# Optimization experiments

Hardware: AMD Instinct MI355X
Metric: run time of the kernel (lower is better)

Reference implementation:

```python
import jax, jax.numpy as jnp
import numpy as np

B, C_LOW, C_HIGH, KC, VC, H, W = 4, 512, 256, 64, 64, 64, 64


def setup_inputs() -> dict:
    key = jax.random.key(0)
    ks = jax.random.split(key, 6)
    x_low = jax.random.normal(ks[0], (B, C_LOW, H, W), dtype=jnp.float32)
    x_high = jax.random.normal(ks[1], (B, C_HIGH, H, W), dtype=jnp.float32)
    # 1x1 conv weights, fan-in scaled
    Wq = jax.random.normal(ks[2], (KC, C_HIGH), dtype=jnp.float32) / np.sqrt(C_HIGH)
    Wk = jax.random.normal(ks[3], (KC, C_LOW), dtype=jnp.float32) / np.sqrt(C_LOW)
    Wv = jax.random.normal(ks[4], (VC, C_LOW), dtype=jnp.float32) / np.sqrt(C_LOW)
    Wo = jax.random.normal(ks[5], (C_HIGH, VC), dtype=jnp.float32) / np.sqrt(VC)
    return {
        "x_low": x_low, "x_high": x_high,
        "Wq": Wq, "bq": jnp.zeros((KC,), jnp.float32),
        "Wk": Wk, "bk": jnp.zeros((KC,), jnp.float32),
        "Wv": Wv, "bv": jnp.zeros((VC,), jnp.float32),
        "Wo": Wo, "bo": jnp.zeros((C_HIGH,), jnp.float32),
    }


def reference(x_low, x_high, Wq, bq, Wk, bk, Wv, bv, Wo, bo):
    b, ch, h, w = x_high.shape
    n = h * w  # tokens per image
    # 1x1 convs == per-pixel linear maps; flatten spatial to tokens
    xh = x_high.reshape(b, ch, n)                # [B, C_high, N]
    xl = x_low.reshape(b, x_low.shape[1], n)     # [B, C_low,  N]
    q = jnp.einsum('kc,bcn->bnk', Wq, xh) + bq   # [B, N, KC]
    k = jnp.einsum('kc,bcn->bkn', Wk, xl) + bk[:, None]  # [B, KC, N]
    v = jnp.einsum('vc,bcn->bnv', Wv, xl) + bv   # [B, N, VC]
    sim = jnp.einsum('bnk,bkm->bnm', q, k)       # [B, N, N]
    attn = jax.nn.softmax(sim, axis=-1)
    ctx = jnp.einsum('bnm,bmv->bnv', attn, v)    # [B, N, VC]
    out = jnp.einsum('ov,bnv->bon', Wo, ctx) + bo[:, None]  # [B, C_high, N]
    return out.reshape(b, ch, h, w) + x_high
```

## Files before the change

### kernel.cpp

```cpp
#include <hip/hip_runtime.h>
#include <hip/hip_bf16.h>
#include <math.h>
#include <stdint.h>

#define B 4
#define CLOW 512
#define CHIGH 256
#define KC 64
#define VC 64
#define N 4096

typedef __attribute__((ext_vector_type(8))) short bf16x8;
typedef __attribute__((ext_vector_type(4))) short bf16x4;
typedef __attribute__((ext_vector_type(4))) float f32x4;

__device__ inline unsigned short f2bf(float f) {
    union { float f; uint32_t u; } v; v.f = f;
    uint32_t u = v.u;
    u += 0x7fff + ((u >> 16) & 1);
    return (unsigned short)(u >> 16);
}
__device__ inline float bf2f(unsigned short h) {
    union { uint32_t u; float f; } v; v.u = ((uint32_t)h) << 16;
    return v.f;
}
__device__ inline uint32_t packbf2(float a, float b) {
    union { __hip_bfloat16 h; unsigned short u; } ca, cb;
    ca.h = __float2bfloat16(a);
    cb.h = __float2bfloat16(b);
    return (uint32_t)ca.u | ((uint32_t)cb.u << 16);
}

#if __has_builtin(__builtin_amdgcn_exp2f)
#define EXP2(x) __builtin_amdgcn_exp2f(x)
#else
#define EXP2(x) exp2f(x)
#endif


__global__ __launch_bounds__(256) void proj_mfma(
    const float* __restrict__ xl, const float* __restrict__ xh,
    const float* __restrict__ Wq, const float* __restrict__ bq,
    const float* __restrict__ Wk, const float* __restrict__ bk,
    const float* __restrict__ Wv, const float* __restrict__ bv,
    unsigned short* __restrict__ Qt, unsigned short* __restrict__ Kt,
    unsigned short* __restrict__ Vt)
{
    const int proj = blockIdx.z;
    const int b    = blockIdx.y;
    const int n0   = blockIdx.x * 64;
    const int tid  = threadIdx.x;
    const int wv   = tid >> 6;
    const int lane = tid & 63;
    const int lo   = lane & 15;
    const int hi   = lane >> 4;
    const int hi8  = hi * 8;

    __shared__ unsigned short XtHi[64][40];
    __shared__ unsigned short XtLo[64][40];

    const int cR = tid >> 3;
    const int t8 = (tid & 7) * 8;

    const size_t kqFragOff = (size_t)((((wv*2 + (hi>>1)) & 3)*16 + lo)*8 + (hi&1)*4);

    if (proj == 0) {
        f32x4 acc[4];
        #pragma unroll
        for (int t = 0; t < 4; ++t)
            #pragma unroll
            for (int r = 0; r < 4; ++r) acc[t][r] = bq[wv*16 + hi*4 + r];

        for (int c0 = 0; c0 < CHIGH; c0 += 32) {
            const float* src = xh + ((size_t)b*CHIGH + c0 + cR)*N + n0 + t8;
            float4 v0 = *(const float4*)src;
            float4 v1 = *(const float4*)(src + 4);
            float vv[8] = {v0.x, v0.y, v0.z, v0.w, v1.x, v1.y, v1.z, v1.w};
            #pragma unroll
            for (int i = 0; i < 8; ++i) {
                unsigned short h = f2bf(vv[i]);
                XtHi[t8 + i][cR] = h;
                XtLo[t8 + i][cR] = f2bf(vv[i] - bf2f(h));
            }
            __syncthreads();

            const float* wp = Wq + (size_t)(wv*16 + lo)*CHIGH + c0 + hi8;
            float4 w0 = *(const float4*)wp;
            float4 w1 = *(const float4*)(wp + 4);
            float ww[8] = {w0.x, w0.y, w0.z, w0.w, w1.x, w1.y, w1.z, w1.w};
            bf16x8 ah, al;
            #pragma unroll
            for (int i = 0; i < 8; ++i) {
                unsigned short h = f2bf(ww[i]);
                ah[i] = (short)h;
                al[i] = (short)f2bf(ww[i] - bf2f(h));
            }

            #pragma unroll
            for (int t = 0; t < 4; ++t) {
                bf16x8 xhv = *(const bf16x8*)&XtHi[t*16 + lo][hi8];
                bf16x8 xlv = *(const bf16x8*)&XtLo[t*16 + lo][hi8];
                acc[t] = __builtin_amdgcn_mfma_f32_16x16x32_bf16(ah, xhv, acc[t], 0, 0, 0);
                acc[t] = __builtin_amdgcn_mfma_f32_16x16x32_bf16(ah, xlv, acc[t], 0, 0, 0);
                acc[t] = __builtin_amdgcn_mfma_f32_16x16x32_bf16(al, xhv, acc[t], 0, 0, 0);
            }
            __syncthreads();
        }
        const float qs = 1.4426950408889634f;
        #pragma unroll
        for (int t = 0; t < 4; ++t) {
            bf16x4 o;
            #pragma unroll
            for (int r = 0; r < 4; ++r) o[r] = (short)f2bf(acc[t][r] * qs);
            size_t base = (((size_t)b*256 + (n0>>4) + t)*2 + (wv>>1))*512;
            *(bf16x4*)&Qt[base + kqFragOff] = o;
        }
    } else {
        f32x4 accK[4], accV[4];
        #pragma unroll
        for (int t = 0; t < 4; ++t)
            #pragma unroll
            for (int r = 0; r < 4; ++r) {
                accK[t][r] = bk[wv*16 + hi*4 + r];
                accV[t][r] = bv[wv*16 + hi*4 + r];
            }

        for (int c0 = 0; c0 < CLOW; c0 += 32) {
            const float* src = xl + ((size_t)b*CLOW + c0 + cR)*N + n0 + t8;
            float4 v0 = *(const float4*)src;
            float4 v1 = *(const float4*)(src + 4);
            float vv[8] = {v0.x, v0.y, v0.z, v0.w, v1.x, v1.y, v1.z, v1.w};
            #pragma unroll
            for (int i = 0; i < 8; ++i) {
                unsigned short h = f2bf(vv[i]);
                XtHi[t8 + i][cR] = h;
                XtLo[t8 + i][cR] = f2bf(vv[i] - bf2f(h));
            }
            __syncthreads();

            const float* wpk = Wk + (size_t)(wv*16 + lo)*CLOW + c0 + hi8;
            const float* wpv = Wv + (size_t)(wv*16 + lo)*CLOW + c0 + hi8;
            bf16x8 ahk, alk, ahv, alv;
            {
                float4 w0 = *(const float4*)wpk;
                float4 w1 = *(const float4*)(wpk + 4);
                float ww[8] = {w0.x,w0.y,w0.z,w0.w,w1.x,w1.y,w1.z,w1.w};
                #pragma unroll
                for (int i = 0; i < 8; ++i) {
                    unsigned short h = f2bf(ww[i]);
                    ahk[i] = (short)h;
                    alk[i] = (short)f2bf(ww[i] - bf2f(h));
                }
            }
            {
                float4 w0 = *(const float4*)wpv;
                float4 w1 = *(const float4*)(wpv + 4);
                float ww[8] = {w0.x,w0.y,w0.z,w0.w,w1.x,w1.y,w1.z,w1.w};
                #pragma unroll
                for (int i = 0; i < 8; ++i) {
                    unsigned short h = f2bf(ww[i]);
                    ahv[i] = (short)h;
                    alv[i] = (short)f2bf(ww[i] - bf2f(h));
                }
            }

            #pragma unroll
            for (int t = 0; t < 4; ++t) {
                bf16x8 xhv = *(const bf16x8*)&XtHi[t*16 + lo][hi8];
                bf16x8 xlv = *(const bf16x8*)&XtLo[t*16 + lo][hi8];
                accK[t] = __builtin_amdgcn_mfma_f32_16x16x32_bf16(ahk, xhv, accK[t], 0, 0, 0);
                accK[t] = __builtin_amdgcn_mfma_f32_16x16x32_bf16(ahk, xlv, accK[t], 0, 0, 0);
                accK[t] = __builtin_amdgcn_mfma_f32_16x16x32_bf16(alk, xhv, accK[t], 0, 0, 0);
                accV[t] = __builtin_amdgcn_mfma_f32_16x16x32_bf16(ahv, xhv, accV[t], 0, 0, 0);
                accV[t] = __builtin_amdgcn_mfma_f32_16x16x32_bf16(ahv, xlv, accV[t], 0, 0, 0);
                accV[t] = __builtin_amdgcn_mfma_f32_16x16x32_bf16(alv, xhv, accV[t], 0, 0, 0);
            }
            __syncthreads();
        }

        #pragma unroll
        for (int t = 0; t < 4; ++t) {
            bf16x4 o;
            #pragma unroll
            for (int r = 0; r < 4; ++r) o[r] = (short)f2bf(accK[t][r]);
            size_t kbase = (((size_t)b*256 + (n0>>4) + t)*2 + (wv>>1))*512;
            *(bf16x4*)&Kt[kbase + kqFragOff] = o;

            const int kvtile = (n0 >> 5) + (t >> 1);
            const int hi_f   = (t & 1)*2 + (lo >> 3);
            size_t vbase = ((size_t)b*128 + kvtile)*2048 + (size_t)wv*512
                         + (size_t)hi_f*128 + (size_t)(lo & 7);
            #pragma unroll
            for (int r = 0; r < 4; ++r)
                Vt[vbase + (size_t)(hi*4 + r)*8] = f2bf(accV[t][r]);
        }
    }
}

#define WSPLIT 8
#define QT 4
__global__ __launch_bounds__(512) void attn(
    const unsigned short* __restrict__ Qt,
    const unsigned short* __restrict__ Kt,
    const unsigned short* __restrict__ Vt,
    float* __restrict__ ctx)
{
    const int bid = blockIdx.x;
    const int xcd = bid & 7;
    const int b   = xcd >> 1;
    const int q0  = ((bid >> 3) * 2 + (xcd & 1)) * 64;

    const int tid  = threadIdx.x;
    const int wv   = tid >> 6;
    const int lane = tid & 63;
    const int lo   = lane & 15;
    const int hi   = lane >> 4;

    __shared__ float Olds[WSPLIT][64][68];
    __shared__ float llds[WSPLIT][64];

    const unsigned short* Kb = Kt + (size_t)b*N*KC;
    const unsigned short* Vb = Vt + (size_t)b*VC*N;
    const unsigned short* Qb = Qt + (size_t)b*N*KC;

    bf16x8 qf[2][QT];
    #pragma unroll
    for (int qt = 0; qt < QT; ++qt) {
        #pragma unroll
        for (int kt = 0; kt < 2; ++kt)
            qf[kt][qt] = *(const bf16x8*)&Qb[(((size_t)(q0>>4) + qt)*2 + kt)*512 + lane*8];
    }

    f32x4 O[4][QT] = {};
    float l_run[QT] = {};

    const int kv0   = wv * (N/WSPLIT);
    const int kvend = kv0 + (N/WSPLIT);

    for (int kv = kv0; kv < kvend; kv += 32) {
        bf16x8 ka[2][2], va[4];
        #pragma unroll
        for (int j = 0; j < 2; ++j)
            #pragma unroll
            for (int m = 0; m < 2; ++m)
                ka[j][m] = *(const bf16x8*)&Kb[(((size_t)(kv>>4) + j)*2 + m)*512 + lane*8];
        #pragma unroll
        for (int vt = 0; vt < 4; ++vt)
            va[vt] = *(const bf16x8*)&Vb[((size_t)(kv>>5))*2048 + vt*512 + lane*8];

        #pragma unroll
        for (int qt = 0; qt < QT; ++qt) {
            f32x4 st[2];
            #pragma unroll
            for (int j = 0; j < 2; ++j) {
                f32x4 z = {};
                z     = __builtin_amdgcn_mfma_f32_16x16x32_bf16(ka[j][0], qf[0][qt], z, 0, 0, 0);
                st[j] = __builtin_amdgcn_mfma_f32_16x16x32_bf16(ka[j][1], qf[1][qt], z, 0, 0, 0);
            }
            uint32_t pk[2][2];
            #pragma unroll
            for (int j = 0; j < 2; ++j) {
                float p0 = EXP2(st[j][0]);
                float p1 = EXP2(st[j][1]);
                float p2 = EXP2(st[j][2]);
                float p3 = EXP2(st[j][3]);
                l_run[qt] += (p0 + p1) + (p2 + p3);
                pk[j][0] = packbf2(p0, p1);
                pk[j][1] = packbf2(p2, p3);
            }
            union { int w[4]; bf16x8 v; } pa;
            #pragma unroll
            for (int w = 0; w < 4; ++w) {
                int src = (2*(hi & 1) + (w >> 1))*16 + lo;
                int t0 = __shfl((int)pk[0][w & 1], src);
                int t1 = __shfl((int)pk[1][w & 1], src);
                pa.w[w] = (hi < 2) ? t0 : t1;
            }
            #pragma unroll
            for (int vt = 0; vt < 4; ++vt)
                O[vt][qt] = __builtin_amdgcn_mfma_f32_16x16x32_bf16(pa.v, va[vt], O[vt][qt], 0, 0, 0);
        }
    }

    #pragma unroll
    for (int qt = 0; qt < QT; ++qt) {
        float s = l_run[qt];
        s += __shfl_xor(s, 16);
        s += __shfl_xor(s, 32);
        l_run[qt] = s;
    }

    #pragma unroll
    for (int qt = 0; qt < QT; ++qt) {
        #pragma unroll
        for (int vt = 0; vt < 4; ++vt)
            #pragma unroll
            for (int r = 0; r < 4; ++r)
                Olds[wv][qt*16 + hi*4 + r][vt*16 + lo] = O[vt][qt][r];
        if (lane < 16) llds[wv][qt*16 + lo] = l_run[qt];
    }
    __syncthreads();

    {
        const int row = tid >> 3;
        const int c8  = (tid & 7) * 8;
        float L = 0.f;
        #pragma unroll
        for (int w = 0; w < WSPLIT; ++w) L += llds[w][row];
        float4 a0 = {0.f,0.f,0.f,0.f}, a1 = {0.f,0.f,0.f,0.f};
        #pragma unroll
        for (int w = 0; w < WSPLIT; ++w) {
            float4 o0 = *(const float4*)&Olds[w][row][c8];
            float4 o1 = *(const float4*)&Olds[w][row][c8 + 4];
            a0.x += o0.x; a0.y += o0.y; a0.z += o0.z; a0.w += o0.w;
            a1.x += o1.x; a1.y += o1.y; a1.z += o1.z; a1.w += o1.w;
        }
        float rL = 1.0f / L;
        a0.x *= rL; a0.y *= rL; a0.z *= rL; a0.w *= rL;
        a1.x *= rL; a1.y *= rL; a1.z *= rL; a1.w *= rL;
        float* cp = &ctx[((size_t)b*N + q0 + row)*VC + c8];
        *(float4*)(cp)     = a0;
        *(float4*)(cp + 4) = a1;
    }
}

__global__ __launch_bounds__(256) void oproj_mfma(
    const float* __restrict__ ctx, const float* __restrict__ Wo,
    const float* __restrict__ bo, const float* __restrict__ xh,
    float* __restrict__ out)
{
    const int b    = blockIdx.y;
    const int n0   = blockIdx.x * 64;
    const int tid  = threadIdx.x;
    const int wv   = tid >> 6;
    const int lane = tid & 63;
    const int lo   = lane & 15;
    const int hi   = lane >> 4;
    const int hi8  = hi * 8;

    for (int tt = 0; tt < 4; ++tt) {
        bf16x8 bh[2], bl[2];
        const float* cp = ctx + ((size_t)b*N + n0 + tt*16 + lo)*VC + hi8;
        #pragma unroll
        for (int j = 0; j < 2; ++j) {
            float4 c0 = *(const float4*)(cp + j*32);
            float4 c1 = *(const float4*)(cp + j*32 + 4);
            float cc[8] = {c0.x,c0.y,c0.z,c0.w,c1.x,c1.y,c1.z,c1.w};
            #pragma unroll
            for (int i = 0; i < 8; ++i) {
                unsigned short h = f2bf(cc[i]);
                bh[j][i] = (short)h;
                bl[j][i] = (short)f2bf(cc[i] - bf2f(h));
            }
        }
        #pragma unroll
        for (int ct = 0; ct < 4; ++ct) {
            const int chan0 = wv*64 + ct*16;
            bf16x8 ah[2], al[2];
            const float* wp = Wo + (size_t)(chan0 + lo)*VC + hi8;
            #pragma unroll
            for (int j = 0; j < 2; ++j) {
                float4 w0 = *(const float4*)(wp + j*32);
                float4 w1 = *(const float4*)(wp + j*32 + 4);
                float ww[8] = {w0.x,w0.y,w0.z,w0.w,w1.x,w1.y,w1.z,w1.w};
                #pragma unroll
                for (int i = 0; i < 8; ++i) {
                    unsigned short h = f2bf(ww[i]);
                    ah[j][i] = (short)h;
                    al[j][i] = (short)f2bf(ww[i] - bf2f(h));
                }
            }
            f32x4 acc;
            #pragma unroll
            for (int r = 0; r < 4; ++r) acc[r] = bo[chan0 + hi*4 + r];
            #pragma unroll
            for (int j = 0; j < 2; ++j) {
                acc = __builtin_amdgcn_mfma_f32_16x16x32_bf16(ah[j], bh[j], acc, 0, 0, 0);
                acc = __builtin_amdgcn_mfma_f32_16x16x32_bf16(ah[j], bl[j], acc, 0, 0, 0);
                acc = __builtin_amdgcn_mfma_f32_16x16x32_bf16(al[j], bh[j], acc, 0, 0, 0);
            }
            #pragma unroll
            for (int r = 0; r < 4; ++r) {
                size_t idx = ((size_t)b*CHIGH + chan0 + hi*4 + r)*N + n0 + tt*16 + lo;
                out[idx] = acc[r] + xh[idx];
            }
        }
    }
}

extern "C" void kernel_launch(void* const* d_in, const int* in_sizes, int n_in,
                              void* d_out, int out_size, void* d_ws, size_t ws_size,
                              hipStream_t stream) {
    const float* xl = (const float*)d_in[0];
    const float* xh = (const float*)d_in[1];
    const float* Wq = (const float*)d_in[2];
    const float* bq = (const float*)d_in[3];
    const float* Wk = (const float*)d_in[4];
    const float* bk = (const float*)d_in[5];
    const float* Wv = (const float*)d_in[6];
    const float* bv = (const float*)d_in[7];
    const float* Wo = (const float*)d_in[8];
    const float* bo = (const float*)d_in[9];
    float* out = (float*)d_out;

    unsigned short* Qt = (unsigned short*)d_ws;
    unsigned short* Kt = Qt + (size_t)B*N*KC;
    unsigned short* Vt = Kt + (size_t)B*N*KC;
    float*         ctxp = (float*)(Vt + (size_t)B*VC*N);

    hipLaunchKernelGGL(proj_mfma, dim3(N/64, B, 2), dim3(256), 0, stream,
                       xl, xh, Wq, bq, Wk, bk, Wv, bv, Qt, Kt, Vt);
    hipLaunchKernelGGL(attn, dim3(256), dim3(512), 0, stream,
                       Qt, Kt, Vt, ctxp);
    hipLaunchKernelGGL(oproj_mfma, dim3(N/64, B), dim3(256), 0, stream,
                       ctxp, Wo, bo, xh, out);
}
```

Measured before the change: 76.97 us.

## Prefetch next channel slab, widen K-step to 64, swizzle LDS in projection kernel

The projection kernel now processes 64 input channels per LDS stage instead of 32, halving the number of barriers. It loads the next slab of activations into registers while MFMAs run on the current one. LDS columns are XOR-swizzled to cut bank conflicts on the transposed stores and fragment reads. The bf16 hi/lo split now goes through the hardware-intrinsic float-to-bf16 conversion, and this is also applied in the output-projection kernel. The cost is more registers for the prefetch buffers and a larger LDS footprint, which may reduce occupancy.

```diff
diff --git a/kernel.cpp b/kernel.cpp
--- a/kernel.cpp
+++ b/kernel.cpp
@@ -30,6 +30,12 @@
     cb.h = __float2bfloat16(b);
     return (uint32_t)ca.u | ((uint32_t)cb.u << 16);
 }
+__device__ inline void bfsplit(float x, short* hi, short* lo) {
+    union { __hip_bfloat16 h; unsigned short u; } c, d;
+    c.h = __float2bfloat16(x);
+    d.h = __float2bfloat16(x - __bfloat162float(c.h));
+    *hi = (short)c.u; *lo = (short)d.u;
+}
 
 #if __has_builtin(__builtin_amdgcn_exp2f)
 #define EXP2(x) __builtin_amdgcn_exp2f(x)
@@ -38,6 +44,7 @@
 #endif
 
 
+#define CSTEP 64
 __global__ __launch_bounds__(256) void proj_mfma(
     const float* __restrict__ xl, const float* __restrict__ xh,
     const float* __restrict__ Wq, const float* __restrict__ bq,
@@ -56,11 +63,57 @@
     const int hi   = lane >> 4;
     const int hi8  = hi * 8;
 
-    __shared__ unsigned short XtHi[64][40];
-    __shared__ unsigned short XtLo[64][40];
-
+    __shared__ unsigned short XtHi[64][72];
+    __shared__ unsigned short XtLo[64][72];
+
+    const int tS = tid & 7;
+    const int t8 = tS * 8;
     const int cR = tid >> 3;
-    const int t8 = (tid & 7) * 8;
+
+    const float* X; int C;
+    if (proj == 0) { X = xh; C = CHIGH; } else { X = xl; C = CLOW; }
+
+    float4 pf[2][2];
+
+    #define LOADX(C0)                                                            \
+        {                                                                        \
+            _Pragma("unroll")                                                    \
+            for (int s = 0; s < 2; ++s) {                                        \
+                const float* src = X + ((size_t)b*C + (C0) + cR + 32*s)*N + n0 + t8; \
+                pf[s][0] = *(const float4*)src;                                  \
+                pf[s][1] = *(const float4*)(src + 4);                            \
+            }                                                                    \
+        }
+
+    #define STAGE()                                                              \
+        {                                                                        \
+            _Pragma("unroll")                                                    \
+            for (int s = 0; s < 2; ++s) {                                        \
+                const int colx = (cR + 32*s) ^ (tS << 3);                        \
+                float vv[8] = {pf[s][0].x, pf[s][0].y, pf[s][0].z, pf[s][0].w,   \
+                               pf[s][1].x, pf[s][1].y, pf[s][1].z, pf[s][1].w};  \
+                _Pragma("unroll")                                                \
+                for (int i = 0; i < 8; ++i) {                                    \
+                    short h_, l_;                                                \
+                    bfsplit(vv[i], &h_, &l_);                                    \
+                    XtHi[t8 + i][colx] = (unsigned short)h_;                     \
+                    XtLo[t8 + i][colx] = (unsigned short)l_;                     \
+                }                                                                \
+            }                                                                    \
+        }
+
+    #define WSPLITLD(WP, AH, AL)                                                 \
+        {                                                                        \
+            float4 w0 = *(const float4*)(WP);                                    \
+            float4 w1 = *(const float4*)((WP) + 4);                              \
+            float ww[8] = {w0.x,w0.y,w0.z,w0.w,w1.x,w1.y,w1.z,w1.w};             \
+            _Pragma("unroll")                                                    \
+            for (int i = 0; i < 8; ++i) {                                        \
+                short h_, l_;                                                    \
+                bfsplit(ww[i], &h_, &l_);                                        \
+                AH[i] = h_; AL[i] = l_;                                          \
+            }                                                                    \
+        }
 
     const size_t kqFragOff = (size_t)((((wv*2 + (hi>>1)) & 3)*16 + lo)*8 + (hi&1)*4);
 
@@ -71,38 +124,26 @@
             #pragma unroll
             for (int r = 0; r < 4; ++r) acc[t][r] = bq[wv*16 + hi*4 + r];
 
-        for (int c0 = 0; c0 < CHIGH; c0 += 32) {
-            const float* src = xh + ((size_t)b*CHIGH + c0 + cR)*N + n0 + t8;
-            float4 v0 = *(const float4*)src;
-            float4 v1 = *(const float4*)(src + 4);
-            float vv[8] = {v0.x, v0.y, v0.z, v0.w, v1.x, v1.y, v1.z, v1.w};
-            #pragma unroll
-            for (int i = 0; i < 8; ++i) {
-                unsigned short h = f2bf(vv[i]);
-                XtHi[t8 + i][cR] = h;
-                XtLo[t8 + i][cR] = f2bf(vv[i] - bf2f(h));
-            }
+        LOADX(0)
+        for (int c0 = 0; c0 < CHIGH; c0 += CSTEP) {
+            STAGE()
             __syncthreads();
-
-            const float* wp = Wq + (size_t)(wv*16 + lo)*CHIGH + c0 + hi8;
-            float4 w0 = *(const float4*)wp;
-            float4 w1 = *(const float4*)(wp + 4);
-            float ww[8] = {w0.x, w0.y, w0.z, w0.w, w1.x, w1.y, w1.z, w1.w};
-            bf16x8 ah, al;
-            #pragma unroll
-            for (int i = 0; i < 8; ++i) {
-                unsigned short h = f2bf(ww[i]);
-                ah[i] = (short)h;
-                al[i] = (short)f2bf(ww[i] - bf2f(h));
-            }
-
-            #pragma unroll
-            for (int t = 0; t < 4; ++t) {
-                bf16x8 xhv = *(const bf16x8*)&XtHi[t*16 + lo][hi8];
-                bf16x8 xlv = *(const bf16x8*)&XtLo[t*16 + lo][hi8];
-                acc[t] = __builtin_amdgcn_mfma_f32_16x16x32_bf16(ah, xhv, acc[t], 0, 0, 0);
-                acc[t] = __builtin_amdgcn_mfma_f32_16x16x32_bf16(ah, xlv, acc[t], 0, 0, 0);
-                acc[t] = __builtin_amdgcn_mfma_f32_16x16x32_bf16(al, xhv, acc[t], 0, 0, 0);
+            if (c0 + CSTEP < CHIGH) LOADX(c0 + CSTEP)
+
+            #pragma unroll
+            for (int m = 0; m < 2; ++m) {
+                bf16x8 ah, al;
+                const float* wp = Wq + (size_t)(wv*16 + lo)*CHIGH + c0 + m*32 + hi8;
+                WSPLITLD(wp, ah, al)
+                #pragma unroll
+                for (int tt = 0; tt < 4; ++tt) {
+                    const int cx = (m*32 + hi8) ^ ((2*tt + (lo >> 3)) << 3);
+                    bf16x8 xhv = *(const bf16x8*)&XtHi[tt*16 + lo][cx];
+                    bf16x8 xlv = *(const bf16x8*)&XtLo[tt*16 + lo][cx];
+                    acc[tt] = __builtin_amdgcn_mfma_f32_16x16x32_bf16(ah, xhv, acc[tt], 0, 0, 0);
+                    acc[tt] = __builtin_amdgcn_mfma_f32_16x16x32_bf16(ah, xlv, acc[tt], 0, 0, 0);
+                    acc[tt] = __builtin_amdgcn_mfma_f32_16x16x32_bf16(al, xhv, acc[tt], 0, 0, 0);
+                }
             }
             __syncthreads();
         }
@@ -125,55 +166,31 @@
                 accV[t][r] = bv[wv*16 + hi*4 + r];
             }
 
-        for (int c0 = 0; c0 < CLOW; c0 += 32) {
-            const float* src = xl + ((size_t)b*CLOW + c0 + cR)*N + n0 + t8;
-            float4 v0 = *(const float4*)src;
-            float4 v1 = *(const float4*)(src + 4);
-            float vv[8] = {v0.x, v0.y, v0.z, v0.w, v1.x, v1.y, v1.z, v1.w};
-            #pragma unroll
-            for (int i = 0; i < 8; ++i) {
-                unsigned short h = f2bf(vv[i]);
-                XtHi[t8 + i][cR] = h;
-                XtLo[t8 + i][cR] = f2bf(vv[i] - bf2f(h));
-            }
+        LOADX(0)
+        for (int c0 = 0; c0 < CLOW; c0 += CSTEP) {
+            STAGE()
             __syncthreads();
-
-            const float* wpk = Wk + (size_t)(wv*16 + lo)*CLOW + c0 + hi8;
-            const float* wpv = Wv + (size_t)(wv*16 + lo)*CLOW + c0 + hi8;
-            bf16x8 ahk, alk, ahv, alv;
-            {
-                float4 w0 = *(const float4*)wpk;
-                float4 w1 = *(const float4*)(wpk + 4);
-                float ww[8] = {w0.x,w0.y,w0.z,w0.w,w1.x,w1.y,w1.z,w1.w};
+            if (c0 + CSTEP < CLOW) LOADX(c0 + CSTEP)
+
+            #pragma unroll
+            for (int m = 0; m < 2; ++m) {
+                bf16x8 ahk, alk, ahv, alv;
+                const float* wpk = Wk + (size_t)(wv*16 + lo)*CLOW + c0 + m*32 + hi8;
+                const float* wpv = Wv + (size_t)(wv*16 + lo)*CLOW + c0 + m*32 + hi8;
+                WSPLITLD(wpk, ahk, alk)
+                WSPLITLD(wpv, ahv, alv)
                 #pragma unroll
-                for (int i = 0; i < 8; ++i) {
-                    unsigned short h = f2bf(ww[i]);
-                    ahk[i] = (short)h;
-                    alk[i] = (short)f2bf(ww[i] - bf2f(h));
+                for (int tt = 0; tt < 4; ++tt) {
+                    const int cx = (m*32 + hi8) ^ ((2*tt + (lo >> 3)) << 3);
+                    bf16x8 xhv = *(const bf16x8*)&XtHi[tt*16 + lo][cx];
+                    bf16x8 xlv = *(const bf16x8*)&XtLo[tt*16 + lo][cx];
+                    accK[tt] = __builtin_amdgcn_mfma_f32_16x16x32_bf16(ahk, xhv, accK[tt], 0, 0, 0);
+                    accK[tt] = __builtin_amdgcn_mfma_f32_16x16x32_bf16(ahk, xlv, accK[tt], 0, 0, 0);
+                    accK[tt] = __builtin_amdgcn_mfma_f32_16x16x32_bf16(alk, xhv, accK[tt], 0, 0, 0);
+                    accV[tt] = __builtin_amdgcn_mfma_f32_16x16x32_bf16(ahv, xhv, accV[tt], 0, 0, 0);
+                    accV[tt] = __builtin_amdgcn_mfma_f32_16x16x32_bf16(ahv, xlv, accV[tt], 0, 0, 0);
+                    accV[tt] = __builtin_amdgcn_mfma_f32_16x16x32_bf16(alv, xhv, accV[tt], 0, 0, 0);
                 }
-            }
-            {
-                float4 w0 = *(const float4*)wpv;
-                float4 w1 = *(const float4*)(wpv + 4);
-                float ww[8] = {w0.x,w0.y,w0.z,w0.w,w1.x,w1.y,w1.z,w1.w};
-                #pragma unroll
-                for (int i = 0; i < 8; ++i) {
-                    unsigned short h = f2bf(ww[i]);
-                    ahv[i] = (short)h;
-                    alv[i] = (short)f2bf(ww[i] - bf2f(h));
-                }
-            }
-
-            #pragma unroll
-            for (int t = 0; t < 4; ++t) {
-                bf16x8 xhv = *(const bf16x8*)&XtHi[t*16 + lo][hi8];
-                bf16x8 xlv = *(const bf16x8*)&XtLo[t*16 + lo][hi8];
-                accK[t] = __builtin_amdgcn_mfma_f32_16x16x32_bf16(ahk, xhv, accK[t], 0, 0, 0);
-                accK[t] = __builtin_amdgcn_mfma_f32_16x16x32_bf16(ahk, xlv, accK[t], 0, 0, 0);
-                accK[t] = __builtin_amdgcn_mfma_f32_16x16x32_bf16(alk, xhv, accK[t], 0, 0, 0);
-                accV[t] = __builtin_amdgcn_mfma_f32_16x16x32_bf16(ahv, xhv, accV[t], 0, 0, 0);
-                accV[t] = __builtin_amdgcn_mfma_f32_16x16x32_bf16(ahv, xlv, accV[t], 0, 0, 0);
-                accV[t] = __builtin_amdgcn_mfma_f32_16x16x32_bf16(alv, xhv, accV[t], 0, 0, 0);
             }
             __syncthreads();
         }
@@ -195,6 +212,9 @@
                 Vt[vbase + (size_t)(hi*4 + r)*8] = f2bf(accV[t][r]);
         }
     }
+    #undef LOADX
+    #undef STAGE
+    #undef WSPLITLD
 }
 
 #define WSPLIT 8
@@ -348,9 +368,10 @@
             float cc[8] = {c0.x,c0.y,c0.z,c0.w,c1.x,c1.y,c1.z,c1.w};
             #pragma unroll
             for (int i = 0; i < 8; ++i) {
-                unsigned short h = f2bf(cc[i]);
-                bh[j][i] = (short)h;
-                bl[j][i] = (short)f2bf(cc[i] - bf2f(h));
+                short h_, l_;
+                bfsplit(cc[i], &h_, &l_);
+                bh[j][i] = h_;
+                bl[j][i] = l_;
             }
         }
         #pragma unroll
@@ -365,9 +386,10 @@
                 float ww[8] = {w0.x,w0.y,w0.z,w0.w,w1.x,w1.y,w1.z,w1.w};
                 #pragma unroll
                 for (int i = 0; i < 8; ++i) {
-                    unsigned short h = f2bf(ww[i]);
-                    ah[j][i] = (short)h;
-                    al[j][i] = (short)f2bf(ww[i] - bf2f(h));
+                    short h_, l_;
+                    bfsplit(ww[i], &h_, &l_);
+                    ah[j][i] = h_;
+                    al[j][i] = l_;
                 }
             }
             f32x4 acc;
```

New measurement: 76.28 us. About the same (-0.9%).
